# Kernel tuning notes

Hardware: AMD Instinct MI355X
Metric: run time of the kernel (lower is better)

The kernel has to match this reference:

```python
import jax, jax.numpy as jnp
import numpy as np

# Module constants (globals in the original source)
N_SPECIAL = 5            # len(SPECIAL_TOKENS)
LABEL_ID = 2             # SPECIAL_TOKENS['<LABEL>']
ACT_VOCAB = 64           # ACTIVITY_VOCAB_SIZE
TIME_VOCAB = 32          # TIME_BUCKET_VOCAB_SIZE
VOCAB = N_SPECIAL + ACT_VOCAB + TIME_VOCAB  # 101


def setup_inputs() -> dict:
    key = jax.random.key(0)
    ks = jax.random.split(key, 8)
    B, T, D = 8, 2048, 1024
    tokens = jax.random.randint(ks[0], (B, T), 0, VOCAB)
    h = jax.random.normal(ks[1], (B, T, D), dtype=jnp.float32)
    E = jax.random.normal(ks[2], (VOCAB, D), dtype=jnp.float32) * 0.02
    W_next = jax.random.normal(ks[3], (ACT_VOCAB, D), dtype=jnp.float32) * (1.0 / np.sqrt(D))
    b_next = jnp.zeros((ACT_VOCAB,), jnp.float32)
    W_time = jax.random.normal(ks[4], (TIME_VOCAB, D), dtype=jnp.float32) * (1.0 / np.sqrt(D))
    b_time = jnp.zeros((TIME_VOCAB,), jnp.float32)
    return {
        'tokens': tokens, 'h': h, 'E': E,
        'W_next': W_next, 'b_next': b_next,
        'W_time': W_time, 'b_time': b_time,
        'tied_scale_act': jnp.asarray(0.0, jnp.float32),
        'tied_scale_time': jnp.asarray(0.0, jnp.float32),
        'copy_scale_act': jnp.asarray(1.5, jnp.float32),
        'copy_scale_time': jnp.asarray(1.5, jnp.float32),
        'copy_temp_act': jnp.asarray(1.0, jnp.float32),
        'copy_temp_time': jnp.asarray(1.0, jnp.float32),
    }


def _heads(tokens, h, E, W_next, b_next, W_time, b_time,
           tied_scale_act, tied_scale_time, copy_scale_act, copy_scale_time,
           copy_temp_act, copy_temp_time):
    act_start = N_SPECIAL
    time_start = N_SPECIAL + ACT_VOCAB
    sp = jax.nn.softplus

    # Parametric heads: [B,T,A], [B,T,Tb]
    param_next = jnp.einsum('btd,ad->bta', h, W_next) + b_next
    param_time = jnp.einsum('btd,cd->btc', h, W_time) + b_time

    # Weight-tied heads from slices of the token-embedding table
    tied_act = jnp.einsum('btd,ad->bta', h, E[act_start:act_start + ACT_VOCAB])
    tied_time = jnp.einsum('btd,cd->btc', h, E[time_start:time_start + TIME_VOCAB])

    # --- Retrieval/copy head, fully vectorized over (b, query, key) ---
    # F.normalize(h, dim=-1) with eps clamp
    hn = h / jnp.maximum(jnp.linalg.norm(h, axis=-1, keepdims=True), 1e-12)
    sims = jnp.einsum('bqd,bkd->bqk', hn, hn)  # [B,T,T] cosine sims

    T = tokens.shape[1]
    is_label = tokens == LABEL_ID                           # [B,T] query gate
    value_mask = jnp.pad(is_label[:, :-1], ((0, 0), (1, 0)))  # pos whose prev tok is <LABEL>
    val_act = value_mask & (tokens >= act_start) & (tokens < time_start)
    val_time = value_mask & (tokens >= time_start) & (tokens < time_start + TIME_VOCAB)
    strict_past = jnp.tril(jnp.ones((T, T), bool), -1)      # key k < query q

    def copy_logits(val_mask, class_idx, n_cls, tau):
        m = is_label[:, :, None] & strict_past[None] & val_mask[:, None, :]
        s = jnp.where(m, sims, 0.0) * tau                   # masked, scaled sims
        onehot = jax.nn.one_hot(jnp.clip(class_idx, 0, n_cls - 1), n_cls, dtype=h.dtype)
        # segment-sum into class buckets: [B,q,k] @ [B,k,c] -> [B,q,c]
        return jnp.einsum('bqk,bkc->bqc', s, onehot)

    copy_act = copy_logits(val_act, tokens - act_start, ACT_VOCAB, sp(copy_temp_act))
    copy_time = copy_logits(val_time, tokens - time_start, TIME_VOCAB, sp(copy_temp_time))

    activity_logits = param_next + sp(tied_scale_act) * tied_act + sp(copy_scale_act) * copy_act
    time_logits = param_time + sp(tied_scale_time) * tied_time + sp(copy_scale_time) * copy_time
    return activity_logits, time_logits


def reference(tokens, h, E, W_next, b_next, W_time, b_time,
              tied_scale_act, tied_scale_time, copy_scale_act, copy_scale_time,
              copy_temp_act, copy_temp_time):
    return _heads(tokens, h, E, W_next, b_next, W_time, b_time,
                  tied_scale_act, tied_scale_time, copy_scale_act, copy_scale_time,
                  copy_temp_act, copy_temp_time)
```

## Files before the change

### kernel.cpp

```cpp
#include <hip/hip_runtime.h>
#include <hip/hip_bf16.h>

#define BATCH  8
#define T_TOK  2048
#define DMODEL 1024
#define BT     (BATCH * T_TOK)
#define NCOLS  96
#define KSPLIT 4
#define KQ     256

typedef __bf16 bf16x8 __attribute__((ext_vector_type(8)));
typedef float  f32x4  __attribute__((ext_vector_type(4)));
typedef unsigned short u16x8 __attribute__((ext_vector_type(8)));

union AB { u16x8 u; bf16x8 b; unsigned int w[4]; };

__device__ __forceinline__ unsigned short f2bf(float f) {
    unsigned u = __float_as_uint(f);
    unsigned r = (u + 0x7fffu + ((u >> 16) & 1u)) >> 16;
    return (unsigned short)r;
}
__device__ __forceinline__ float softplusf(float x) {
    return fmaxf(x, 0.f) + log1pf(expf(-fabsf(x)));
}
__device__ __forceinline__ float wave_sum(float v) {
#pragma unroll
    for (int o = 32; o > 0; o >>= 1) v += __shfl_xor(v, o, 64);
    return v;
}
__device__ __forceinline__ unsigned int pack_rtz(float lo, float hi) {
    return __builtin_amdgcn_perm(__float_as_uint(hi), __float_as_uint(lo), 0x07060302u);
}
__device__ __forceinline__ void atomic_fadd(float* p, float v) {
    unsafeAtomicAdd(p, v);
}
__device__ __forceinline__ void async16(const void* g, void* l) {
    __builtin_amdgcn_global_load_lds(
        (const __attribute__((address_space(1))) unsigned int*)g,
        (__attribute__((address_space(3))) unsigned int*)l, 16, 0, 0);
}

__global__ __launch_bounds__(256) void prep_init_kernel(
    const float* __restrict__ E,
    const float* __restrict__ Wn,
    const float* __restrict__ bn,
    const float* __restrict__ Wt,
    const float* __restrict__ bt,
    const float* __restrict__ tsa,
    const float* __restrict__ tst,
    unsigned short* __restrict__ Weff,
    float* __restrict__ out)
{
    const int blk = blockIdx.x;
    if (blk < 384) {
        int idx = blk * 256 + threadIdx.x;
        int row = idx >> 10, k = idx & 1023;
        float w;
        if (row < 64) {
            w = Wn[idx] + softplusf(tsa[0]) * E[(5 + row) * 1024 + k];
        } else {
            int c = row - 64;
            w = Wt[c * 1024 + k] + softplusf(tst[0]) * E[(69 + c) * 1024 + k];
        }
        Weff[idx] = f2bf(w);
    } else {
        int i = (blk - 384) * 256 + threadIdx.x;
        if (i < 262144) {
            float4 b = reinterpret_cast<const float4*>(bn)[i & 15];
            reinterpret_cast<float4*>(out)[i] = b;
        } else {
            int k = i - 262144;
            float4 b = reinterpret_cast<const float4*>(bt)[k & 7];
            reinterpret_cast<float4*>(out)[i] = b;
        }
    }
}

__global__ __launch_bounds__(256, 3) void gemm_kernel(
    const float* __restrict__ h,
    const unsigned short* __restrict__ Weff,
    float* __restrict__ out)
{
    __shared__ float4 Bbuf[3072];

    const int tid  = threadIdx.x;
    const int lane = tid & 63;
    const int wave = tid >> 6;
    const int m = lane & 15;
    const int q = lane >> 4;
    const int tok0 = blockIdx.x * 64;
    const int kq   = blockIdx.y;

    const float* hrow = h + (size_t)(tok0 + wave * 16 + m) * DMODEL + kq * KQ;
    float4 areg[16];
#pragma unroll
    for (int kw = 0; kw < 8; ++kw) {
        areg[kw * 2]     = *reinterpret_cast<const float4*>(hrow + kw * 32 + q * 8);
        areg[kw * 2 + 1] = *reinterpret_cast<const float4*>(hrow + kw * 32 + q * 8 + 4);
    }

#pragma unroll
    for (int i = 0; i < 12; ++i) {
        int u = i * 256 + tid;
        int row = u >> 5, c = u & 31;
        async16(Weff + (size_t)row * DMODEL + kq * KQ + ((c ^ (row & 7)) << 3),
                &Bbuf[u]);
    }
    __syncthreads();

    f32x4 acc[6];
#pragma unroll
    for (int n = 0; n < 6; ++n) acc[n] = (f32x4){0.f, 0.f, 0.f, 0.f};

    const int s = m & 7;
#pragma unroll
    for (int kw = 0; kw < 8; ++kw) {
        float4 f0 = areg[kw * 2];
        float4 f1 = areg[kw * 2 + 1];
        AB a;
        a.w[0] = pack_rtz(f0.x, f0.y);
        a.w[1] = pack_rtz(f0.z, f0.w);
        a.w[2] = pack_rtz(f1.x, f1.y);
        a.w[3] = pack_rtz(f1.z, f1.w);
        const int cu = kw * 4 + q;
#pragma unroll
        for (int n = 0; n < 6; ++n) {
            const int rb = n * 16 + m;
            const bf16x8* bp = reinterpret_cast<const bf16x8*>(
                &Bbuf[rb * 32 + (cu ^ s)]);
            acc[n] = __builtin_amdgcn_mfma_f32_16x16x32_bf16(a.b, *bp, acc[n], 0, 0, 0);
        }
    }

#pragma unroll
    for (int n = 0; n < 6; ++n) {
        const int j = n * 16 + m;
#pragma unroll
        for (int rr = 0; rr < 4; ++rr) {
            const int t = tok0 + wave * 16 + q * 4 + rr;
            float* dst = (j < 64) ? &out[(size_t)t * 64 + j]
                                  : &out[(size_t)BT * 64 + (size_t)t * 32 + (j - 64)];
            atomic_fadd(dst, acc[n][rr]);
        }
    }
}

__global__ __launch_bounds__(1024) void copy_kernel(
    const int* __restrict__ tokens,
    const float* __restrict__ h,
    const float* __restrict__ csa,
    const float* __restrict__ cst,
    const float* __restrict__ cta,
    const float* __restrict__ ctt,
    float* __restrict__ out)
{
    const int b     = blockIdx.x >> 3;
    const int slice = blockIdx.x & 7;
    const int tid  = threadIdx.x;
    const int wave = tid >> 6, lane = tid & 63;

    __shared__ int cnt_q[32], cnt_k[32], off_q[32], off_k[32];
    __shared__ int s_nq, s_nk;
    __shared__ int   q_pos[T_TOK];
    __shared__ int   k_pos[T_TOK];
    __shared__ int   k_col[T_TOK];
    __shared__ float q_nrm[T_TOK];
    __shared__ float k_nrm[T_TOK];

    const int* tk = tokens + b * T_TOK;

#pragma unroll
    for (int c = 0; c < 2; ++c) {
        int chunk = wave * 2 + c;
        int t = chunk * 64 + lane;
        int v = tk[t];
        bool pq = (v == 2);
        bool pk = (t > 0) && (tk[t - 1] == 2) && (v >= 5) && (v < 101);
        unsigned long long mq = __ballot(pq);
        unsigned long long mk = __ballot(pk);
        if (lane == 0) { cnt_q[chunk] = __popcll(mq); cnt_k[chunk] = __popcll(mk); }
    }
    __syncthreads();
    if (tid == 0) {
        int aq = 0, ak = 0;
        for (int i = 0; i < 32; ++i) {
            off_q[i] = aq; aq += cnt_q[i];
            off_k[i] = ak; ak += cnt_k[i];
        }
        s_nq = aq; s_nk = ak;
    }
    __syncthreads();

#pragma unroll
    for (int c = 0; c < 2; ++c) {
        int chunk = wave * 2 + c;
        int t = chunk * 64 + lane;
        int v = tk[t];
        bool pq = (v == 2);
        bool pk = (t > 0) && (tk[t - 1] == 2) && (v >= 5) && (v < 101);
        unsigned long long mq = __ballot(pq);
        unsigned long long mk = __ballot(pk);
        unsigned long long below = (lane == 0) ? 0ull : ((~0ull) >> (64 - lane));
        if (pq) q_pos[off_q[chunk] + __popcll(mq & below)] = t;
        if (pk) {
            int i = off_k[chunk] + __popcll(mk & below);
            k_pos[i] = t;
            k_col[i] = (v < 69) ? (v - 5) : (64 + (v - 69));
        }
    }
    __syncthreads();
    const int nq = s_nq, nk = s_nk;
    const float* hb = h + (size_t)b * T_TOK * DMODEL;

    for (int i = wave; i < nq + nk; i += 16) {
        const int row = (i < nq) ? q_pos[i] : k_pos[i - nq];
        const float4* p = reinterpret_cast<const float4*>(hb + (size_t)row * DMODEL);
        float ssum = 0.f;
#pragma unroll
        for (int c = 0; c < 4; ++c) {
            float4 v = p[lane + c * 64];
            ssum += v.x * v.x + v.y * v.y + v.z * v.z + v.w * v.w;
        }
        ssum = wave_sum(ssum);
        if (lane == 0) {
            float nn = fmaxf(sqrtf(ssum), 1e-12f);
            if (i < nq) q_nrm[i] = nn; else k_nrm[i - nq] = nn;
        }
    }
    __syncthreads();

    const float fa = softplusf(csa[0]) * softplusf(cta[0]);
    const float ft = softplusf(cst[0]) * softplusf(ctt[0]);
    const int P = nq * nk;
    const int g = slice * 16 + wave;
    for (int p = g; p < P; p += 128) {
        const int qi = p / nk, ki = p - qi * nk;
        const int qp = q_pos[qi], kp = k_pos[ki];
        if (kp >= qp) continue;
        const float4* pq = reinterpret_cast<const float4*>(hb + (size_t)qp * DMODEL);
        const float4* pk = reinterpret_cast<const float4*>(hb + (size_t)kp * DMODEL);
        float ssum = 0.f;
#pragma unroll
        for (int c = 0; c < 4; ++c) {
            float4 va = pq[lane + c * 64];
            float4 vb = pk[lane + c * 64];
            ssum += va.x * vb.x + va.y * vb.y + va.z * vb.z + va.w * vb.w;
        }
        ssum = wave_sum(ssum);
        if (lane == 0) {
            const int col = k_col[ki];
            const float val = ((col < 64) ? fa : ft) * (ssum / (q_nrm[qi] * k_nrm[ki]));
            const size_t tg = (size_t)b * T_TOK + qp;
            float* dst = (col < 64) ? &out[tg * 64 + col]
                                    : &out[(size_t)BT * 64 + tg * 32 + (col - 64)];
            atomic_fadd(dst, val);
        }
    }
}

extern "C" void kernel_launch(void* const* d_in, const int* in_sizes, int n_in,
                              void* d_out, int out_size, void* d_ws, size_t ws_size,
                              hipStream_t stream) {
    const int* tokens = (const int*)d_in[0];
    const float* h    = (const float*)d_in[1];
    const float* E    = (const float*)d_in[2];
    const float* Wn   = (const float*)d_in[3];
    const float* bn   = (const float*)d_in[4];
    const float* Wt   = (const float*)d_in[5];
    const float* bt   = (const float*)d_in[6];
    const float* tsa  = (const float*)d_in[7];
    const float* tst  = (const float*)d_in[8];
    const float* csa  = (const float*)d_in[9];
    const float* cst  = (const float*)d_in[10];
    const float* cta  = (const float*)d_in[11];
    const float* ctt  = (const float*)d_in[12];

    unsigned short* Weff = (unsigned short*)d_ws;
    float* out           = (float*)d_out;

    prep_init_kernel<<<dim3(1920), dim3(256), 0, stream>>>(E, Wn, bn, Wt, bt, tsa, tst, Weff, out);
    gemm_kernel<<<dim3(BT / 64, KSPLIT), dim3(256), 0, stream>>>(h, Weff, out);
    copy_kernel<<<dim3(64), dim3(1024), 0, stream>>>(tokens, h, csa, cst, cta, ctt, out);
}
```

Before: 147.7 us.

## Replace split-K atomics with in-block K reduction and direct weight loads

```diff
diff --git a/kernel.cpp b/kernel.cpp
--- a/kernel.cpp
+++ b/kernel.cpp
@@ -6,8 +6,6 @@
 #define DMODEL 1024
 #define BT     (BATCH * T_TOK)
 #define NCOLS  96
-#define KSPLIT 4
-#define KQ     256
 
 typedef __bf16 bf16x8 __attribute__((ext_vector_type(8)));
 typedef float  f32x4  __attribute__((ext_vector_type(4)));
@@ -34,13 +32,8 @@
 __device__ __forceinline__ void atomic_fadd(float* p, float v) {
     unsafeAtomicAdd(p, v);
 }
-__device__ __forceinline__ void async16(const void* g, void* l) {
-    __builtin_amdgcn_global_load_lds(
-        (const __attribute__((address_space(1))) unsigned int*)g,
-        (__attribute__((address_space(3))) unsigned int*)l, 16, 0, 0);
-}
-
-__global__ __launch_bounds__(256) void prep_init_kernel(
+
+__global__ __launch_bounds__(256) void prep_kernel(
     const float* __restrict__ E,
     const float* __restrict__ Wn,
     const float* __restrict__ bn,
@@ -49,49 +42,37 @@
     const float* __restrict__ tsa,
     const float* __restrict__ tst,
     unsigned short* __restrict__ Weff,
-    float* __restrict__ out)
+    float* __restrict__ beff)
 {
-    const int blk = blockIdx.x;
-    if (blk < 384) {
-        int idx = blk * 256 + threadIdx.x;
-        int row = idx >> 10, k = idx & 1023;
-        float w;
-        if (row < 64) {
-            w = Wn[idx] + softplusf(tsa[0]) * E[(5 + row) * 1024 + k];
-        } else {
-            int c = row - 64;
-            w = Wt[c * 1024 + k] + softplusf(tst[0]) * E[(69 + c) * 1024 + k];
-        }
-        Weff[idx] = f2bf(w);
+    int idx = blockIdx.x * 256 + threadIdx.x;
+    int row = idx >> 10, k = idx & 1023;
+    float w;
+    if (row < 64) {
+        w = Wn[idx] + softplusf(tsa[0]) * E[(5 + row) * 1024 + k];
     } else {
-        int i = (blk - 384) * 256 + threadIdx.x;
-        if (i < 262144) {
-            float4 b = reinterpret_cast<const float4*>(bn)[i & 15];
-            reinterpret_cast<float4*>(out)[i] = b;
-        } else {
-            int k = i - 262144;
-            float4 b = reinterpret_cast<const float4*>(bt)[k & 7];
-            reinterpret_cast<float4*>(out)[i] = b;
-        }
-    }
+        int c = row - 64;
+        w = Wt[c * 1024 + k] + softplusf(tst[0]) * E[(69 + c) * 1024 + k];
+    }
+    Weff[idx] = f2bf(w);
+    if (k == 0) beff[row] = (row < 64) ? bn[row] : bt[row - 64];
 }
 
 __global__ __launch_bounds__(256, 3) void gemm_kernel(
     const float* __restrict__ h,
     const unsigned short* __restrict__ Weff,
+    const float* __restrict__ beff,
     float* __restrict__ out)
 {
-    __shared__ float4 Bbuf[3072];
+    __shared__ float red[4 * 1536];
 
     const int tid  = threadIdx.x;
     const int lane = tid & 63;
     const int wave = tid >> 6;
     const int m = lane & 15;
     const int q = lane >> 4;
-    const int tok0 = blockIdx.x * 64;
-    const int kq   = blockIdx.y;
-
-    const float* hrow = h + (size_t)(tok0 + wave * 16 + m) * DMODEL + kq * KQ;
+    const int tok0 = blockIdx.x * 16;
+
+    const float* hrow = h + (size_t)(tok0 + m) * DMODEL + wave * 256;
     float4 areg[16];
 #pragma unroll
     for (int kw = 0; kw < 8; ++kw) {
@@ -99,20 +80,11 @@
         areg[kw * 2 + 1] = *reinterpret_cast<const float4*>(hrow + kw * 32 + q * 8 + 4);
     }
 
-#pragma unroll
-    for (int i = 0; i < 12; ++i) {
-        int u = i * 256 + tid;
-        int row = u >> 5, c = u & 31;
-        async16(Weff + (size_t)row * DMODEL + kq * KQ + ((c ^ (row & 7)) << 3),
-                &Bbuf[u]);
-    }
-    __syncthreads();
-
     f32x4 acc[6];
 #pragma unroll
     for (int n = 0; n < 6; ++n) acc[n] = (f32x4){0.f, 0.f, 0.f, 0.f};
 
-    const int s = m & 7;
+    const unsigned short* wbase = Weff + (size_t)m * DMODEL + wave * 256;
 #pragma unroll
     for (int kw = 0; kw < 8; ++kw) {
         float4 f0 = areg[kw * 2];
@@ -122,26 +94,32 @@
         a.w[1] = pack_rtz(f0.z, f0.w);
         a.w[2] = pack_rtz(f1.x, f1.y);
         a.w[3] = pack_rtz(f1.z, f1.w);
-        const int cu = kw * 4 + q;
+        const int ko = kw * 32 + q * 8;
 #pragma unroll
         for (int n = 0; n < 6; ++n) {
-            const int rb = n * 16 + m;
-            const bf16x8* bp = reinterpret_cast<const bf16x8*>(
-                &Bbuf[rb * 32 + (cu ^ s)]);
-            acc[n] = __builtin_amdgcn_mfma_f32_16x16x32_bf16(a.b, *bp, acc[n], 0, 0, 0);
-        }
-    }
-
-#pragma unroll
-    for (int n = 0; n < 6; ++n) {
-        const int j = n * 16 + m;
-#pragma unroll
-        for (int rr = 0; rr < 4; ++rr) {
-            const int t = tok0 + wave * 16 + q * 4 + rr;
-            float* dst = (j < 64) ? &out[(size_t)t * 64 + j]
-                                  : &out[(size_t)BT * 64 + (size_t)t * 32 + (j - 64)];
-            atomic_fadd(dst, acc[n][rr]);
-        }
+            bf16x8 bfrag = *reinterpret_cast<const bf16x8*>(wbase + (size_t)n * 16 * DMODEL + ko);
+            acc[n] = __builtin_amdgcn_mfma_f32_16x16x32_bf16(a.b, bfrag, acc[n], 0, 0, 0);
+        }
+    }
+
+    float* myred = red + wave * 1536;
+#pragma unroll
+    for (int n = 0; n < 6; ++n)
+#pragma unroll
+        for (int r = 0; r < 4; ++r)
+            myred[(q * 4 + r) * 96 + n * 16 + m] = acc[n][r];
+    __syncthreads();
+
+#pragma unroll
+    for (int i = 0; i < 6; ++i) {
+        const int idx = i * 256 + tid;
+        float v = red[idx] + red[1536 + idx] + red[3072 + idx] + red[4608 + idx];
+        const int tl  = idx / 96;
+        const int col = idx - tl * 96;
+        v += beff[col];
+        const int t = tok0 + tl;
+        if (col < 64) out[(size_t)t * 64 + col] = v;
+        else          out[(size_t)BT * 64 + (size_t)t * 32 + (col - 64)] = v;
     }
 }
 
@@ -275,10 +253,12 @@
     const float* cta  = (const float*)d_in[11];
     const float* ctt  = (const float*)d_in[12];
 
-    unsigned short* Weff = (unsigned short*)d_ws;
+    char* ws = (char*)d_ws;
+    float* beff          = (float*)ws;
+    unsigned short* Weff = (unsigned short*)(ws + 1024);
     float* out           = (float*)d_out;
 
-    prep_init_kernel<<<dim3(1920), dim3(256), 0, stream>>>(E, Wn, bn, Wt, bt, tsa, tst, Weff, out);
-    gemm_kernel<<<dim3(BT / 64, KSPLIT), dim3(256), 0, stream>>>(h, Weff, out);
+    prep_kernel<<<dim3(384), dim3(256), 0, stream>>>(E, Wn, bn, Wt, bt, tsa, tst, Weff, beff);
+    gemm_kernel<<<dim3(BT / 16), dim3(256), 0, stream>>>(h, Weff, beff, out);
     copy_kernel<<<dim3(64), dim3(1024), 0, stream>>>(tokens, h, csa, cst, cta, ctt, out);
 }
```

After: 156.3 us. 1.06x slower.
